# Performance work log

Hardware: AMD Instinct MI355X
Metric: run time of the kernel (lower is better)

Reference implementation:

```python
import math
import jax, jax.numpy as jnp
import numpy as np

N_LAYERS = 3

def _layer_masks(d):
    # Deterministic reproduction of generate_mask_matrix: mask_ratio = 0 for
    # layer < 2 else 1 - log(1/layer + 1); int(ratio*d) random dims zeroed.
    masks = []
    for layer in range(N_LAYERS):
        ratio = 0.0 if layer < 2 else 1.0 - math.log(1.0 / layer + 1.0)
        num_masked = int(ratio * d)
        perm = np.random.RandomState(layer).permutation(d)
        masks.append(jnp.asarray((perm >= num_masked).astype(np.float32)))
    return masks


def setup_inputs() -> dict:
    key = jax.random.key(0)
    ks = jax.random.split(key, 12)
    U, I, R, D, E, B = 50000, 50000, 5, 64, 1000000, 8192
    N = U + I
    return {
        "users": jax.random.randint(ks[0], (B,), 0, U, dtype=jnp.int32),
        "items": jax.random.randint(ks[1], (B,), 0, I, dtype=jnp.int32),
        "user_emb": jax.random.normal(ks[2], (U, D), dtype=jnp.float32) * 0.01,
        "item_emb": jax.random.normal(ks[3], (I, D), dtype=jnp.float32) * 0.01,
        "rating_emb": jax.random.normal(ks[4], (R, D), dtype=jnp.float32) * 0.01,
        "W1": jax.random.normal(ks[5], (R, 2 * D, D), dtype=jnp.float32) * (1.0 / math.sqrt(2 * D)),
        "b1": jnp.zeros((R, D), dtype=jnp.float32),
        "W2": jax.random.normal(ks[6], (R, D, D), dtype=jnp.float32) * (1.0 / math.sqrt(D)),
        "b2": jnp.zeros((R, D), dtype=jnp.float32),
        "rows": jax.random.randint(ks[7], (R, E), 0, N, dtype=jnp.int32),
        "cols": jax.random.randint(ks[8], (R, E), 0, N, dtype=jnp.int32),
        # normalized-adjacency-like positive values (~1/avg_degree)
        "vals": jax.random.uniform(ks[9], (R, E), dtype=jnp.float32) * 0.1,
    }


def reference(users, items, user_emb, item_emb, rating_emb, W1, b1, W2, b2, rows, cols, vals):
    U = user_emb.shape[0]
    N = U + item_emb.shape[0]
    R, D = rating_emb.shape
    masks = _layer_masks(D)

    base = jnp.concatenate([user_emb, item_emb], axis=0)  # [N, D]
    group_outs = []
    for r in range(R):  # fixed small set of rating groups
        # per-rating attention MLP on cat([emb, rating_emb_r])
        t = jnp.concatenate([base, jnp.broadcast_to(rating_emb[r], (N, D))], axis=1)  # [N, 2D]
        h = jax.nn.leaky_relu(t @ W1[r] + b1[r]) @ W2[r] + b2[r]  # [N, D]
        acc = h
        prev = h
        for layer in range(N_LAYERS):
            # sparse A @ prev via gather + segment_sum
            agg = jax.ops.segment_sum(vals[r][:, None] * prev[cols[r]], rows[r], num_segments=N)
            m = masks[layer]
            prev = agg * m + prev * (1.0 - m)  # diag-mask residual combine
            acc = acc + prev
        group_outs.append(acc)

    out = jnp.mean(jnp.stack(group_outs, axis=1), axis=1)  # agg == 'mean'
    users_emb = out[users]
    items_emb = out[U + items]
    return (users_emb * items_emb).sum(1)  # is_mlp = False
```

## Files before the change

kernel.cpp:

```cpp
#include <hip/hip_runtime.h>
#include <hip/hip_bf16.h>
#include <cstdint>
#include <cstddef>

#define KEYSHIFT 20
#define COLMASK 0xFFFFFu
#define EPB 8192
#define SUB 4096
#define BSHIFT 8
#define NRB 256
#define CCAP 3072

__device__ __forceinline__ unsigned short f2bf(float f) {
    uint32_t u = __float_as_uint(f);
    u += ((u >> 16) & 1u) + 0x7fffu;
    return (unsigned short)(u >> 16);
}
__device__ __forceinline__ float bf2f(unsigned short h) {
    return __uint_as_float(((uint32_t)h) << 16);
}

static uint64_t compute_mask_bits() {
    uint32_t mt[624];
    mt[0] = 2u;
    for (int i = 1; i < 624; i++)
        mt[i] = 1812433253u * (mt[i - 1] ^ (mt[i - 1] >> 30)) + (uint32_t)i;
    int mti = 624;
    auto genrand = [&]() -> uint32_t {
        if (mti >= 624) {
            for (int k = 0; k < 624; k++) {
                uint32_t y = (mt[k] & 0x80000000u) | (mt[(k + 1) % 624] & 0x7fffffffu);
                mt[k] = mt[(k + 397) % 624] ^ (y >> 1) ^ ((y & 1u) ? 2567483615u : 0u);
            }
            mti = 0;
        }
        uint32_t y = mt[mti++];
        y ^= y >> 11;
        y ^= (y << 7) & 2636928640u;
        y ^= (y << 15) & 4022730752u;
        y ^= y >> 18;
        return y;
    };
    int arr[64];
    for (int i = 0; i < 64; i++) arr[i] = i;
    for (int i = 63; i >= 1; i--) {
        uint32_t mask = (uint32_t)i;
        mask |= mask >> 1; mask |= mask >> 2; mask |= mask >> 4;
        mask |= mask >> 8; mask |= mask >> 16;
        uint32_t v;
        do { v = genrand() & mask; } while (v > (uint32_t)i);
        int tmp = arr[i]; arr[i] = arr[v]; arr[v] = tmp;
    }
    uint64_t bits = 0;
    for (int d = 0; d < 64; d++)
        if (arr[d] >= 38) bits |= (1ull << d);
    return bits;
}

__global__ void flag_kernel(const int* __restrict__ users, const int* __restrict__ items,
                            unsigned char* __restrict__ flag, int B, int U) {
    int i = blockIdx.x * 256 + threadIdx.x;
    if (i < B) flag[users[i]] = 1;
    else if (i < 2 * B) flag[U + items[i - B]] = 1;
}

__global__ void flist_kernel(const unsigned char* __restrict__ flag,
                             int* __restrict__ flist, int* __restrict__ fcount, int n) {
    int i = blockIdx.x * 256 + threadIdx.x;
    if (i < n && flag[i]) {
        int p = atomicAdd(fcount, 1);
        flist[p] = i;
    }
}

__global__ void c1_kernel(const float* __restrict__ rating_emb, const float* __restrict__ W1,
                          const float* __restrict__ b1, float* __restrict__ c1_all) {
    int r = blockIdx.x;
    int t = threadIdx.x;
    const float* W1r = W1 + (size_t)r * (128 * 64);
    float acc = b1[r * 64 + t];
    for (int k = 0; k < 64; k++)
        acc += rating_emb[r * 64 + k] * W1r[(64 + k) * 64 + t];
    c1_all[r * 64 + t] = acc;
}

__global__ __launch_bounds__(1024) void bucket_count_kernel(
    const int* __restrict__ rows, int* __restrict__ gcnt,
    int* __restrict__ blockBase, int E, int K, int nb) {
    __shared__ int hist[2048];
    int r = blockIdx.y, blk = blockIdx.x, t = threadIdx.x;
    for (int i = t; i < K; i += 1024) hist[i] = 0;
    __syncthreads();
    size_t base = (size_t)r * E + (size_t)blk * EPB;
    int cnt = E - blk * EPB;
    if (cnt > EPB) cnt = EPB;
    for (int k = t; k < cnt; k += 1024)
        atomicAdd(&hist[rows[base + k] >> BSHIFT], 1);
    __syncthreads();
    for (int i = t; i < K; i += 1024) {
        int c = hist[i];
        int bb = (c > 0) ? atomicAdd(&gcnt[r * K + i], c) : 0;
        blockBase[((size_t)r * nb + blk) * K + i] = bb;
    }
}

__global__ void bucket_scan_kernel(const int* __restrict__ gcnt,
                                   int* __restrict__ bptr, int K) {
    __shared__ int sh[256];
    int r = blockIdx.x;
    int t = threadIdx.x;
    int base = t * 8;
    int v[8];
    int s = 0;
    #pragma unroll
    for (int j = 0; j < 8; j++) {
        int idx = base + j;
        v[j] = (idx < K) ? gcnt[r * K + idx] : 0;
        s += v[j];
    }
    sh[t] = s;
    __syncthreads();
    for (int off = 1; off < 256; off <<= 1) {
        int x = (t >= off) ? sh[t - off] : 0;
        __syncthreads();
        sh[t] += x;
        __syncthreads();
    }
    int run = sh[t] - s;
    #pragma unroll
    for (int j = 0; j < 8; j++) {
        int idx = base + j;
        if (idx <= K) bptr[r * (K + 1) + idx] = run;
        run += v[j];
    }
}

__global__ __launch_bounds__(1024) void bucket_scatter_kernel(
    const int* __restrict__ rows, const int* __restrict__ cols,
    const float* __restrict__ vals, const int* __restrict__ bptr,
    const int* __restrict__ blockBase, uint2* __restrict__ rec,
    int E, int K, long long eStride, long long pStride,
    long long bbStride, long long rStride) {
    __shared__ uint2 staged[SUB];
    __shared__ int gaddr[SUB];
    __shared__ int cursor[512];
    __shared__ int lhist[512];
    __shared__ int aux[512];
    int r = blockIdx.y;
    const int* rows_r = rows + (size_t)r * eStride;
    const int* cols_r = cols + (size_t)r * eStride;
    const float* vals_r = vals + (size_t)r * eStride;
    const int* bptr_r = bptr + (size_t)r * pStride;
    const int* bb_r = blockBase + (size_t)r * bbStride;
    uint2* rec_r = rec + (size_t)r * rStride;
    int blk = blockIdx.x, t = threadIdx.x;
    if (t < 512)
        cursor[t] = (t < K) ? (bptr_r[t] + bb_r[(size_t)blk * K + t]) : 0;
    size_t base = (size_t)blk * EPB;
    int cnt = E - blk * EPB;
    if (cnt > EPB) cnt = EPB;
    for (int c0 = 0; c0 < cnt; c0 += SUB) {
        int scnt = cnt - c0;
        if (scnt > SUB) scnt = SUB;
        if (t < 512) lhist[t] = 0;
        __syncthreads();
        int bkt_[4], lpos_[4];
        uint2 rv_[4];
        #pragma unroll
        for (int q = 0; q < 4; q++) {
            int kk = (q << 10) + t;
            bkt_[q] = -1;
            if (kk < scnt) {
                size_t g = base + c0 + kk;
                int row = rows_r[g];
                int b = row >> BSHIFT;
                bkt_[q] = b;
                rv_[q] = make_uint2(((uint32_t)(row & (NRB - 1)) << KEYSHIFT) |
                                        (uint32_t)cols_r[g],
                                    __float_as_uint(vals_r[g]));
                lpos_[q] = atomicAdd(&lhist[b], 1);
            }
        }
        __syncthreads();
        int v = (t < 512) ? lhist[t] : 0;
        if (t < 512) aux[t] = v;
        __syncthreads();
        for (int off = 1; off < 512; off <<= 1) {
            int x = 0;
            if (t >= off && t < 512) x = aux[t - off];
            __syncthreads();
            if (t < 512) aux[t] += x;
            __syncthreads();
        }
        if (t < 512) {
            int ex = aux[t] - v;
            int gb = cursor[t];
            cursor[t] = gb + v;
            lhist[t] = ex;
            aux[t] = gb - ex;
        }
        __syncthreads();
        #pragma unroll
        for (int q = 0; q < 4; q++) {
            if (bkt_[q] >= 0) {
                int sidx = lhist[bkt_[q]] + lpos_[q];
                staged[sidx] = rv_[q];
                gaddr[sidx] = aux[bkt_[q]] + sidx;
            }
        }
        __syncthreads();
        for (int i = t; i < scnt; i += 1024)
            rec_r[gaddr[i]] = staged[i];
        __syncthreads();
    }
}

__global__ __launch_bounds__(1024) void bucket_scatter_legacy(
    const int* __restrict__ rows, const int* __restrict__ cols,
    const float* __restrict__ vals, const int* __restrict__ bptr,
    const int* __restrict__ blockBase, uint2* __restrict__ rec,
    int E, int K, long long eStride, long long pStride,
    long long bbStride, long long rStride) {
    __shared__ int cursor[2048];
    int r = blockIdx.y;
    const int* rows_r = rows + (size_t)r * eStride;
    const int* cols_r = cols + (size_t)r * eStride;
    const float* vals_r = vals + (size_t)r * eStride;
    const int* bptr_r = bptr + (size_t)r * pStride;
    const int* bb_r = blockBase + (size_t)r * bbStride;
    uint2* rec_r = rec + (size_t)r * rStride;
    int blk = blockIdx.x, t = threadIdx.x;
    for (int i = t; i < K; i += 1024)
        cursor[i] = bptr_r[i] + bb_r[(size_t)blk * K + i];
    __syncthreads();
    size_t base = (size_t)blk * EPB;
    int cnt = E - blk * EPB;
    if (cnt > EPB) cnt = EPB;
    for (int k = t; k < cnt; k += 1024) {
        int row = rows_r[base + k];
        int b = row >> BSHIFT;
        int pos = atomicAdd(&cursor[b], 1);
        uint32_t key = ((uint32_t)(row & (NRB - 1)) << KEYSHIFT) | (uint32_t)cols_r[base + k];
        rec_r[pos] = make_uint2(key, __float_as_uint(vals_r[base + k]));
    }
}

__global__ __launch_bounds__(256) void bucket_sort_kernel(
    const uint2* __restrict__ rec, uint2* __restrict__ srec,
    const int* __restrict__ bptr, int* __restrict__ rp, int K, int N,
    long long rStride, long long pStride, long long rpStride) {
    __shared__ uint2 staged[CCAP];
    __shared__ int hist[NRB];
    __shared__ int excl[NRB];
    int r = blockIdx.y;
    const uint2* rec_r = rec + (size_t)r * rStride;
    uint2* srec_r = srec + (size_t)r * rStride;
    const int* bptr_r = bptr + (size_t)r * pStride;
    int* rp_r = rp + (size_t)r * rpStride;
    int b = blockIdx.x;
    int t = threadIdx.x;
    hist[t] = 0;
    __syncthreads();
    int start = bptr_r[b], end = bptr_r[b + 1];
    int m = end - start;
    for (int e = start + t; e < end; e += 256)
        atomicAdd(&hist[rec_r[e].x >> KEYSHIFT], 1);
    __syncthreads();
    int v = hist[t];
    excl[t] = v;
    __syncthreads();
    for (int off = 1; off < 256; off <<= 1) {
        int x = (t >= off) ? excl[t - off] : 0;
        __syncthreads();
        excl[t] += x;
        __syncthreads();
    }
    int ex = excl[t] - v;
    excl[t] = ex;
    hist[t] = 0;
    int row = b * NRB + t;
    if (row < N) rp_r[row] = start + ex;
    if (b == K - 1 && t == 0) rp_r[N] = bptr_r[K];
    __syncthreads();
    if (m <= CCAP) {
        for (int e = start + t; e < end; e += 256) {
            uint2 rr = rec_r[e];
            int rel = (int)(rr.x >> KEYSHIFT);
            int pos = excl[rel] + atomicAdd(&hist[rel], 1);
            staged[pos] = rr;
        }
        __syncthreads();
        for (int i = t; i < m; i += 256)
            srec_r[start + i] = staged[i];
    } else {
        for (int e = start + t; e < end; e += 256) {
            uint2 rr = rec_r[e];
            int rel = (int)(rr.x >> KEYSHIFT);
            int pos = start + excl[rel] + atomicAdd(&hist[rel], 1);
            srec_r[pos] = rr;
        }
    }
}

__global__ __launch_bounds__(256, 4) void mlp_kernel(
    const float* __restrict__ user_emb, const float* __restrict__ item_emb,
    const float* __restrict__ W1, const float* __restrict__ W2,
    const float* __restrict__ c1_all, const float* __restrict__ b2,
    unsigned short* __restrict__ prev, long long prevStride,
    float* __restrict__ out_acc, const unsigned char* __restrict__ flag,
    int r0, int nr, int n_rows, int U, int init) {
    __shared__ float sX[64 * 68];
    __shared__ float sT[64 * 68];

    int t = threadIdx.x;
    int lane = t & 63;
    int row0 = blockIdx.x * 64;
    int jbase = __builtin_amdgcn_readfirstlane((t >> 6) << 4);

    #pragma unroll
    for (int q = 0; q < 4; q++) {
        int f = t + 256 * q;
        int i = f >> 4, c = (f & 15) * 4;
        int nrow = row0 + i;
        float4 xv = make_float4(0.f, 0.f, 0.f, 0.f);
        if (nrow < n_rows) {
            const float* src = (nrow < U) ? (user_emb + (size_t)nrow * 64)
                                          : (item_emb + (size_t)(nrow - U) * 64);
            xv = *(const float4*)(src + c);
        }
        *(float4*)(sX + i * 68 + c) = xv;
    }
    __syncthreads();

    int nrow = row0 + lane;
    bool valid = (nrow < n_rows);
    bool fl = valid && flag[nrow];
    float oa[16];
    #pragma unroll
    for (int i = 0; i < 16; i++) oa[i] = 0.f;

    for (int rr = r0; rr < r0 + nr; ++rr) {
        const float* W1r = W1 + (size_t)rr * (128 * 64);
        const float* W2r = W2 + (size_t)rr * (64 * 64);

        const float* c1p = c1_all + rr * 64 + jbase;
        float4 a0 = *(const float4*)(c1p + 0);
        float4 a1 = *(const float4*)(c1p + 4);
        float4 a2 = *(const float4*)(c1p + 8);
        float4 a3 = *(const float4*)(c1p + 12);

        #pragma unroll
        for (int m = 0; m < 16; m++) {
            float4 xv = *(const float4*)(sX + lane * 68 + 4 * m);
            const float* wk = W1r + (4 * m) * 64 + jbase;
            #pragma unroll
            for (int kk = 0; kk < 4; kk++) {
                float xs = (kk == 0) ? xv.x : (kk == 1) ? xv.y : (kk == 2) ? xv.z : xv.w;
                float4 w0 = *(const float4*)(wk + kk * 64 + 0);
                float4 w1 = *(const float4*)(wk + kk * 64 + 4);
                float4 w2 = *(const float4*)(wk + kk * 64 + 8);
                float4 w3 = *(const float4*)(wk + kk * 64 + 12);
                a0.x += xs * w0.x; a0.y += xs * w0.y; a0.z += xs * w0.z; a0.w += xs * w0.w;
                a1.x += xs * w1.x; a1.y += xs * w1.y; a1.z += xs * w1.z; a1.w += xs * w1.w;
                a2.x += xs * w2.x; a2.y += xs * w2.y; a2.z += xs * w2.z; a2.w += xs * w2.w;
                a3.x += xs * w3.x; a3.y += xs * w3.y; a3.z += xs * w3.z; a3.w += xs * w3.w;
            }
        }
        a0.x = (a0.x >= 0.f) ? a0.x : 0.01f * a0.x;
        a0.y = (a0.y >= 0.f) ? a0.y : 0.01f * a0.y;
        a0.z = (a0.z >= 0.f) ? a0.z : 0.01f * a0.z;
        a0.w = (a0.w >= 0.f) ? a0.w : 0.01f * a0.w;
        a1.x = (a1.x >= 0.f) ? a1.x : 0.01f * a1.x;
        a1.y = (a1.y >= 0.f) ? a1.y : 0.01f * a1.y;
        a1.z = (a1.z >= 0.f) ? a1.z : 0.01f * a1.z;
        a1.w = (a1.w >= 0.f) ? a1.w : 0.01f * a1.w;
        a2.x = (a2.x >= 0.f) ? a2.x : 0.01f * a2.x;
        a2.y = (a2.y >= 0.f) ? a2.y : 0.01f * a2.y;
        a2.z = (a2.z >= 0.f) ? a2.z : 0.01f * a2.z;
        a2.w = (a2.w >= 0.f) ? a2.w : 0.01f * a2.w;
        a3.x = (a3.x >= 0.f) ? a3.x : 0.01f * a3.x;
        a3.y = (a3.y >= 0.f) ? a3.y : 0.01f * a3.y;
        a3.z = (a3.z >= 0.f) ? a3.z : 0.01f * a3.z;
        a3.w = (a3.w >= 0.f) ? a3.w : 0.01f * a3.w;

        *(float4*)(sT + lane * 68 + jbase + 0) = a0;
        *(float4*)(sT + lane * 68 + jbase + 4) = a1;
        *(float4*)(sT + lane * 68 + jbase + 8) = a2;
        *(float4*)(sT + lane * 68 + jbase + 12) = a3;
        __syncthreads();

        const float* b2p = b2 + rr * 64 + jbase;
        a0 = *(const float4*)(b2p + 0);
        a1 = *(const float4*)(b2p + 4);
        a2 = *(const float4*)(b2p + 8);
        a3 = *(const float4*)(b2p + 12);

        #pragma unroll
        for (int m = 0; m < 16; m++) {
            float4 xv = *(const float4*)(sT + lane * 68 + 4 * m);
            const float* wk = W2r + (4 * m) * 64 + jbase;
            #pragma unroll
            for (int kk = 0; kk < 4; kk++) {
                float xs = (kk == 0) ? xv.x : (kk == 1) ? xv.y : (kk == 2) ? xv.z : xv.w;
                float4 w0 = *(const float4*)(wk + kk * 64 + 0);
                float4 w1 = *(const float4*)(wk + kk * 64 + 4);
                float4 w2 = *(const float4*)(wk + kk * 64 + 8);
                float4 w3 = *(const float4*)(wk + kk * 64 + 12);
                a0.x += xs * w0.x; a0.y += xs * w0.y; a0.z += xs * w0.z; a0.w += xs * w0.w;
                a1.x += xs * w1.x; a1.y += xs * w1.y; a1.z += xs * w1.z; a1.w += xs * w1.w;
                a2.x += xs * w2.x; a2.y += xs * w2.y; a2.z += xs * w2.z; a2.w += xs * w2.w;
                a3.x += xs * w3.x; a3.y += xs * w3.y; a3.z += xs * w3.z; a3.w += xs * w3.w;
            }
        }

        if (valid) {
            unsigned short* pp = prev + (size_t)rr * prevStride
                               + (size_t)nrow * 64 + jbase;
            ushort4 h0, h1, h2, h3;
            h0.x = f2bf(a0.x); h0.y = f2bf(a0.y); h0.z = f2bf(a0.z); h0.w = f2bf(a0.w);
            h1.x = f2bf(a1.x); h1.y = f2bf(a1.y); h1.z = f2bf(a1.z); h1.w = f2bf(a1.w);
            h2.x = f2bf(a2.x); h2.y = f2bf(a2.y); h2.z = f2bf(a2.z); h2.w = f2bf(a2.w);
            h3.x = f2bf(a3.x); h3.y = f2bf(a3.y); h3.z = f2bf(a3.z); h3.w = f2bf(a3.w);
            *(ushort4*)(pp + 0) = h0;
            *(ushort4*)(pp + 4) = h1;
            *(ushort4*)(pp + 8) = h2;
            *(ushort4*)(pp + 12) = h3;
            if (fl) {
                oa[0] += a0.x;  oa[1] += a0.y;  oa[2] += a0.z;  oa[3] += a0.w;
                oa[4] += a1.x;  oa[5] += a1.y;  oa[6] += a1.z;  oa[7] += a1.w;
                oa[8] += a2.x;  oa[9] += a2.y;  oa[10] += a2.z; oa[11] += a2.w;
                oa[12] += a3.x; oa[13] += a3.y; oa[14] += a3.z; oa[15] += a3.w;
            }
        }
        __syncthreads();
    }

    if (fl) {
        float* o = out_acc + (size_t)nrow * 64 + jbase;
        if (init) {
            *(float4*)(o + 0) = make_float4(oa[0], oa[1], oa[2], oa[3]);
            *(float4*)(o + 4) = make_float4(oa[4], oa[5], oa[6], oa[7]);
            *(float4*)(o + 8) = make_float4(oa[8], oa[9], oa[10], oa[11]);
            *(float4*)(o + 12) = make_float4(oa[12], oa[13], oa[14], oa[15]);
        } else {
            float4 o0 = *(const float4*)(o + 0);
            float4 o1 = *(const float4*)(o + 4);
            float4 o2 = *(const float4*)(o + 8);
            float4 o3 = *(const float4*)(o + 12);
            o0.x += oa[0];  o0.y += oa[1];  o0.z += oa[2];  o0.w += oa[3];
            o1.x += oa[4];  o1.y += oa[5];  o1.z += oa[6];  o1.w += oa[7];
            o2.x += oa[8];  o2.y += oa[9];  o2.z += oa[10]; o2.w += oa[11];
            o3.x += oa[12]; o3.y += oa[13]; o3.z += oa[14]; o3.w += oa[15];
            *(float4*)(o + 0) = o0;
            *(float4*)(o + 4) = o1;
            *(float4*)(o + 8) = o2;
            *(float4*)(o + 12) = o3;
        }
    }
}

__global__ __launch_bounds__(256) void spmm_kernel(
    const unsigned short* __restrict__ prev, unsigned short* __restrict__ next,
    float* __restrict__ out_acc, const int* __restrict__ rp,
    const uint2* __restrict__ rec, const unsigned char* __restrict__ flag, int n) {
    int wave = (int)((blockIdx.x * (unsigned)blockDim.x + threadIdx.x) >> 6);
    int lane = threadIdx.x & 63;
    int rA = wave * 2;
    if (rA >= n) return;
    int rB = rA + 1;
    int sub = lane >> 4;
    int dl = lane & 15;
    int sA = rp[rA], eA = rp[rA + 1];
    int sB = 0, eB = 0;
    if (rB < n) { sB = rp[rB]; eB = rp[rB + 1]; }
    float axA = 0.f, ayA = 0.f, azA = 0.f, awA = 0.f;
    float axB = 0.f, ayB = 0.f, azB = 0.f, awB = 0.f;
    int ewA = sA + sub, ewB = sB + sub;
    while (ewA < eA || ewB < eB) {
        int a1 = ewA + 4, a2 = ewA + 8, a3 = ewA + 12;
        int b1 = ewB + 4, b2 = ewB + 8, b3 = ewB + 12;
        uint2 ra0 = rec[ewA < eA ? ewA : 0];
        uint2 ra1 = rec[a1 < eA ? a1 : 0];
        uint2 ra2 = rec[a2 < eA ? a2 : 0];
        uint2 ra3 = rec[a3 < eA ? a3 : 0];
        uint2 rb0 = rec[ewB < eB ? ewB : 0];
        uint2 rb1 = rec[b1 < eB ? b1 : 0];
        uint2 rb2 = rec[b2 < eB ? b2 : 0];
        uint2 rb3 = rec[b3 < eB ? b3 : 0];
        float vA0 = (ewA < eA) ? __uint_as_float(ra0.y) : 0.f;
        float vA1 = (a1 < eA) ? __uint_as_float(ra1.y) : 0.f;
        float vA2 = (a2 < eA) ? __uint_as_float(ra2.y) : 0.f;
        float vA3 = (a3 < eA) ? __uint_as_float(ra3.y) : 0.f;
        float vB0 = (ewB < eB) ? __uint_as_float(rb0.y) : 0.f;
        float vB1 = (b1 < eB) ? __uint_as_float(rb1.y) : 0.f;
        float vB2 = (b2 < eB) ? __uint_as_float(rb2.y) : 0.f;
        float vB3 = (b3 < eB) ? __uint_as_float(rb3.y) : 0.f;
        ushort4 qa0 = *(const ushort4*)(prev + (size_t)(ra0.x & COLMASK) * 64 + dl * 4);
        ushort4 qa1 = *(const ushort4*)(prev + (size_t)(ra1.x & COLMASK) * 64 + dl * 4);
        ushort4 qa2 = *(const ushort4*)(prev + (size_t)(ra2.x & COLMASK) * 64 + dl * 4);
        ushort4 qa3 = *(const ushort4*)(prev + (size_t)(ra3.x & COLMASK) * 64 + dl * 4);
        ushort4 qb0 = *(const ushort4*)(prev + (size_t)(rb0.x & COLMASK) * 64 + dl * 4);
        ushort4 qb1 = *(const ushort4*)(prev + (size_t)(rb1.x & COLMASK) * 64 + dl * 4);
        ushort4 qb2 = *(const ushort4*)(prev + (size_t)(rb2.x & COLMASK) * 64 + dl * 4);
        ushort4 qb3 = *(const ushort4*)(prev + (size_t)(rb3.x & COLMASK) * 64 + dl * 4);
        axA += vA0 * bf2f(qa0.x) + vA1 * bf2f(qa1.x) + vA2 * bf2f(qa2.x) + vA3 * bf2f(qa3.x);
        ayA += vA0 * bf2f(qa0.y) + vA1 * bf2f(qa1.y) + vA2 * bf2f(qa2.y) + vA3 * bf2f(qa3.y);
        azA += vA0 * bf2f(qa0.z) + vA1 * bf2f(qa1.z) + vA2 * bf2f(qa2.z) + vA3 * bf2f(qa3.z);
        awA += vA0 * bf2f(qa0.w) + vA1 * bf2f(qa1.w) + vA2 * bf2f(qa2.w) + vA3 * bf2f(qa3.w);
        axB += vB0 * bf2f(qb0.x) + vB1 * bf2f(qb1.x) + vB2 * bf2f(qb2.x) + vB3 * bf2f(qb3.x);
        ayB += vB0 * bf2f(qb0.y) + vB1 * bf2f(qb1.y) + vB2 * bf2f(qb2.y) + vB3 * bf2f(qb3.y);
        azB += vB0 * bf2f(qb0.z) + vB1 * bf2f(qb1.z) + vB2 * bf2f(qb2.z) + vB3 * bf2f(qb3.z);
        awB += vB0 * bf2f(qb0.w) + vB1 * bf2f(qb1.w) + vB2 * bf2f(qb2.w) + vB3 * bf2f(qb3.w);
        ewA += 16; ewB += 16;
    }
    axA += __shfl_xor(axA, 16); ayA += __shfl_xor(ayA, 16);
    azA += __shfl_xor(azA, 16); awA += __shfl_xor(awA, 16);
    axA += __shfl_xor(axA, 32); ayA += __shfl_xor(ayA, 32);
    azA += __shfl_xor(azA, 32); awA += __shfl_xor(awA, 32);
    axB += __shfl_xor(axB, 16); ayB += __shfl_xor(ayB, 16);
    azB += __shfl_xor(azB, 16); awB += __shfl_xor(awB, 16);
    axB += __shfl_xor(axB, 32); ayB += __shfl_xor(ayB, 32);
    azB += __shfl_xor(azB, 32); awB += __shfl_xor(awB, 32);
    if (sub == 0) {
        ushort4 nv;
        nv.x = f2bf(axA); nv.y = f2bf(ayA); nv.z = f2bf(azA); nv.w = f2bf(awA);
        *(ushort4*)(next + (size_t)rA * 64 + dl * 4) = nv;
    } else if (sub == 1 && flag[rA]) {
        float* o = out_acc + (size_t)rA * 64 + dl * 4;
        float4 ov = *(const float4*)o;
        ov.x += axA; ov.y += ayA; ov.z += azA; ov.w += awA;
        *(float4*)o = ov;
    } else if (sub == 2 && rB < n) {
        ushort4 nv;
        nv.x = f2bf(axB); nv.y = f2bf(ayB); nv.z = f2bf(azB); nv.w = f2bf(awB);
        *(ushort4*)(next + (size_t)rB * 64 + dl * 4) = nv;
    } else if (sub == 3 && rB < n && flag[rB]) {
        float* o = out_acc + (size_t)rB * 64 + dl * 4;
        float4 ov = *(const float4*)o;
        ov.x += axB; ov.y += ayB; ov.z += azB; ov.w += awB;
        *(float4*)o = ov;
    }
}

__global__ __launch_bounds__(256) void spmm_masked_kernel(
    const unsigned short* __restrict__ prev, float* __restrict__ out_acc,
    const int* __restrict__ rp, const uint2* __restrict__ rec,
    unsigned long long maskbits, const int* __restrict__ flist,
    const int* __restrict__ fcount) {
    int wave = (int)((blockIdx.x * (unsigned)blockDim.x + threadIdx.x) >> 6);
    int lane = threadIdx.x & 63;
    int fc = *fcount;
    int w2 = wave * 2;
    if (w2 >= fc) return;
    int rowA = flist[w2];
    int rowB = (w2 + 1 < fc) ? flist[w2 + 1] : -1;
    int sub = lane >> 4;
    int dl = lane & 15;
    int sA = rp[rowA], eA = rp[rowA + 1];
    int sB = 0, eB = 0;
    if (rowB >= 0) { sB = rp[rowB]; eB = rp[rowB + 1]; }
    float axA = 0.f, ayA = 0.f, azA = 0.f, awA = 0.f;
    float axB = 0.f, ayB = 0.f, azB = 0.f, awB = 0.f;
    int ewA = sA + sub, ewB = sB + sub;
    while (ewA < eA || ewB < eB) {
        int a1 = ewA + 4, a2 = ewA + 8, a3 = ewA + 12;
        int b1 = ewB + 4, b2 = ewB + 8, b3 = ewB + 12;
        uint2 ra0 = rec[ewA < eA ? ewA : 0];
        uint2 ra1 = rec[a1 < eA ? a1 : 0];
        uint2 ra2 = rec[a2 < eA ? a2 : 0];
        uint2 ra3 = rec[a3 < eA ? a3 : 0];
        uint2 rb0 = rec[ewB < eB ? ewB : 0];
        uint2 rb1 = rec[b1 < eB ? b1 : 0];
        uint2 rb2 = rec[b2 < eB ? b2 : 0];
        uint2 rb3 = rec[b3 < eB ? b3 : 0];
        float vA0 = (ewA < eA) ? __uint_as_float(ra0.y) : 0.f;
        float vA1 = (a1 < eA) ? __uint_as_float(ra1.y) : 0.f;
        float vA2 = (a2 < eA) ? __uint_as_float(ra2.y) : 0.f;
        float vA3 = (a3 < eA) ? __uint_as_float(ra3.y) : 0.f;
        float vB0 = (ewB < eB) ? __uint_as_float(rb0.y) : 0.f;
        float vB1 = (b1 < eB) ? __uint_as_float(rb1.y) : 0.f;
        float vB2 = (b2 < eB) ? __uint_as_float(rb2.y) : 0.f;
        float vB3 = (b3 < eB) ? __uint_as_float(rb3.y) : 0.f;
        ushort4 qa0 = *(const ushort4*)(prev + (size_t)(ra0.x & COLMASK) * 64 + dl * 4);
        ushort4 qa1 = *(const ushort4*)(prev + (size_t)(ra1.x & COLMASK) * 64 + dl * 4);
        ushort4 qa2 = *(const ushort4*)(prev + (size_t)(ra2.x & COLMASK) * 64 + dl * 4);
        ushort4 qa3 = *(const ushort4*)(prev + (size_t)(ra3.x & COLMASK) * 64 + dl * 4);
        ushort4 qb0 = *(const ushort4*)(prev + (size_t)(rb0.x & COLMASK) * 64 + dl * 4);
        ushort4 qb1 = *(const ushort4*)(prev + (size_t)(rb1.x & COLMASK) * 64 + dl * 4);
        ushort4 qb2 = *(const ushort4*)(prev + (size_t)(rb2.x & COLMASK) * 64 + dl * 4);
        ushort4 qb3 = *(const ushort4*)(prev + (size_t)(rb3.x & COLMASK) * 64 + dl * 4);
        axA += vA0 * bf2f(qa0.x) + vA1 * bf2f(qa1.x) + vA2 * bf2f(qa2.x) + vA3 * bf2f(qa3.x);
        ayA += vA0 * bf2f(qa0.y) + vA1 * bf2f(qa1.y) + vA2 * bf2f(qa2.y) + vA3 * bf2f(qa3.y);
        azA += vA0 * bf2f(qa0.z) + vA1 * bf2f(qa1.z) + vA2 * bf2f(qa2.z) + vA3 * bf2f(qa3.z);
        awA += vA0 * bf2f(qa0.w) + vA1 * bf2f(qa1.w) + vA2 * bf2f(qa2.w) + vA3 * bf2f(qa3.w);
        axB += vB0 * bf2f(qb0.x) + vB1 * bf2f(qb1.x) + vB2 * bf2f(qb2.x) + vB3 * bf2f(qb3.x);
        ayB += vB0 * bf2f(qb0.y) + vB1 * bf2f(qb1.y) + vB2 * bf2f(qb2.y) + vB3 * bf2f(qb3.y);
        azB += vB0 * bf2f(qb0.z) + vB1 * bf2f(qb1.z) + vB2 * bf2f(qb2.z) + vB3 * bf2f(qb3.z);
        awB += vB0 * bf2f(qb0.w) + vB1 * bf2f(qb1.w) + vB2 * bf2f(qb2.w) + vB3 * bf2f(qb3.w);
        ewA += 16; ewB += 16;
    }
    axA += __shfl_xor(axA, 16); ayA += __shfl_xor(ayA, 16);
    azA += __shfl_xor(azA, 16); awA += __shfl_xor(awA, 16);
    axA += __shfl_xor(axA, 32); ayA += __shfl_xor(ayA, 32);
    azA += __shfl_xor(azA, 32); awA += __shfl_xor(awA, 32);
    axB += __shfl_xor(axB, 16); ayB += __shfl_xor(ayB, 16);
    azB += __shfl_xor(azB, 16); awB += __shfl_xor(awB, 16);
    axB += __shfl_xor(axB, 32); ayB += __shfl_xor(ayB, 32);
    azB += __shfl_xor(azB, 32); awB += __shfl_xor(awB, 32);
    if (sub == 0) {
        ushort4 pq = *(const ushort4*)(prev + (size_t)rowA * 64 + dl * 4);
        float px = bf2f(pq.x), py = bf2f(pq.y), pz = bf2f(pq.z), pw = bf2f(pq.w);
        float rx = ((maskbits >> (dl * 4 + 0)) & 1ull) ? axA : px;
        float ry = ((maskbits >> (dl * 4 + 1)) & 1ull) ? ayA : py;
        float rz = ((maskbits >> (dl * 4 + 2)) & 1ull) ? azA : pz;
        float rw = ((maskbits >> (dl * 4 + 3)) & 1ull) ? awA : pw;
        float* o = out_acc + (size_t)rowA * 64 + dl * 4;
        float4 ov = *(const float4*)o;
        ov.x += rx; ov.y += ry; ov.z += rz; ov.w += rw;
        *(float4*)o = ov;
    } else if (sub == 2 && rowB >= 0) {
        ushort4 pq = *(const ushort4*)(prev + (size_t)rowB * 64 + dl * 4);
        float px = bf2f(pq.x), py = bf2f(pq.y), pz = bf2f(pq.z), pw = bf2f(pq.w);
        float rx = ((maskbits >> (dl * 4 + 0)) & 1ull) ? axB : px;
        float ry = ((maskbits >> (dl * 4 + 1)) & 1ull) ? ayB : py;
        float rz = ((maskbits >> (dl * 4 + 2)) & 1ull) ? azB : pz;
        float rw = ((maskbits >> (dl * 4 + 3)) & 1ull) ? awB : pw;
        float* o = out_acc + (size_t)rowB * 64 + dl * 4;
        float4 ov = *(const float4*)o;
        ov.x += rx; ov.y += ry; ov.z += rz; ov.w += rw;
        *(float4*)o = ov;
    }
}

__global__ __launch_bounds__(256) void dot_kernel(
    const float* __restrict__ out_acc, const int* __restrict__ users,
    const int* __restrict__ items, float* __restrict__ out,
    int Bn, int U, float scale) {
    int w = (int)((blockIdx.x * (unsigned)blockDim.x + threadIdx.x) >> 6);
    int lane = threadIdx.x & 63;
    if (w >= Bn) return;
    int u = users[w], it = items[w];
    float a = out_acc[(size_t)u * 64 + lane];
    float c = out_acc[((size_t)(U + it)) * 64 + lane];
    float p = a * c;
    #pragma unroll
    for (int off = 32; off > 0; off >>= 1) p += __shfl_down(p, off);
    if (lane == 0) out[w] = p * scale;
}

extern "C" void kernel_launch(void* const* d_in, const int* in_sizes, int n_in,
                              void* d_out, int out_size, void* d_ws, size_t ws_size,
                              hipStream_t stream) {
    const int* users = (const int*)d_in[0];
    const int* items = (const int*)d_in[1];
    const float* user_emb = (const float*)d_in[2];
    const float* item_emb = (const float*)d_in[3];
    const float* rating_emb = (const float*)d_in[4];
    const float* W1 = (const float*)d_in[5];
    const float* b1 = (const float*)d_in[6];
    const float* W2 = (const float*)d_in[7];
    const float* b2 = (const float*)d_in[8];
    const int* rows = (const int*)d_in[9];
    const int* cols = (const int*)d_in[10];
    const float* vals = (const float*)d_in[11];
    float* out = (float*)d_out;

    const int Dd = 64;
    int U = in_sizes[2] / Dd;
    int I = in_sizes[3] / Dd;
    int R = in_sizes[4] / Dd;
    int N = U + I;
    int E = in_sizes[9] / R;
    int Bn = in_sizes[0];
    int K = (N + NRB - 1) / NRB;
    int nb = (E + EPB - 1) / EPB;

    auto al = [](size_t b) { return (b + 255) & ~(size_t)255; };
    size_t sliceA = al((size_t)N * 64 * 2);
    size_t bufA_all = al((size_t)R * N * 64 * 2);
    size_t common = al((size_t)N * 64 * 4) + sliceA
        + al((size_t)R * K * 4)
        + al((size_t)R * (K + 1) * 4) + al((size_t)R * nb * K * 4)
        + al((size_t)R * (N + 1) * 4) + al((size_t)R * 64 * 4)
        + al((size_t)N) + al((size_t)2 * Bn * 4) + al(4);
    size_t rec_one = al((size_t)E * 8);
    size_t rec_all = al((size_t)E * 8 * R);
    int mlpb = 0, batched = 0;
    if (ws_size >= common + bufA_all + 2 * rec_all + 65536) {
        mlpb = 1; batched = 1;
    } else if (ws_size >= common + sliceA + 2 * rec_all + 65536) {
        batched = 1;
    }
    size_t bufAsz = mlpb ? bufA_all : sliceA;
    size_t recsz = batched ? rec_all : rec_one;

    char* p = (char*)d_ws;
    auto carve = [&](size_t bytes) -> char* {
        char* q = p;
        p += (bytes + 255) & ~(size_t)255;
        return q;
    };
    float* out_acc = (float*)carve((size_t)N * 64 * 4);
    unsigned short* bufA = (unsigned short*)carve(bufAsz);
    unsigned short* bufB = (unsigned short*)carve(sliceA);
    uint2* rec = (uint2*)carve(recsz);
    uint2* srec = (uint2*)carve(recsz);
    int* gcnt = (int*)carve((size_t)R * K * 4);
    int* bptr = (int*)carve((size_t)R * (K + 1) * 4);
    int* blockBase = (int*)carve((size_t)R * nb * K * 4);
    int* row_ptr = (int*)carve((size_t)R * (N + 1) * 4);
    float* c1_all = (float*)carve((size_t)R * 64 * 4);
    unsigned char* flag = (unsigned char*)carve((size_t)N);
    int* flist = (int*)carve((size_t)2 * Bn * 4);
    int* fcount = (int*)carve(4);

    uint64_t maskbits = compute_mask_bits();

    hipMemsetAsync(flag, 0, (size_t)N, stream);
    hipMemsetAsync(fcount, 0, 4, stream);
    hipMemsetAsync(gcnt, 0, (size_t)R * K * 4, stream);

    flag_kernel<<<(2 * Bn + 255) / 256, 256, 0, stream>>>(users, items, flag, Bn, U);
    flist_kernel<<<(N + 255) / 256, 256, 0, stream>>>(flag, flist, fcount, N);
    c1_kernel<<<R, 64, 0, stream>>>(rating_emb, W1, b1, c1_all);

    dim3 cgrid(nb, R);
    bucket_count_kernel<<<cgrid, 1024, 0, stream>>>(rows, gcnt, blockBase, E, K, nb);
    bucket_scan_kernel<<<R, 256, 0, stream>>>(gcnt, bptr, K);

    if (batched) {
        dim3 sgrid(nb, R);
        if (K <= 512)
            bucket_scatter_kernel<<<sgrid, 1024, 0, stream>>>(
                rows, cols, vals, bptr, blockBase, rec, E, K,
                (long long)E, (long long)(K + 1), (long long)nb * K, (long long)E);
        else
            bucket_scatter_legacy<<<sgrid, 1024, 0, stream>>>(
                rows, cols, vals, bptr, blockBase, rec, E, K,
                (long long)E, (long long)(K + 1), (long long)nb * K, (long long)E);
        dim3 ogrid(K, R);
        bucket_sort_kernel<<<ogrid, 256, 0, stream>>>(
            rec, srec, bptr, row_ptr, K, N,
            (long long)E, (long long)(K + 1), (long long)(N + 1));
    }

    if (mlpb)
        mlp_kernel<<<(N + 63) / 64, 256, 0, stream>>>(
            user_emb, item_emb, W1, W2, c1_all, b2,
            bufA, (long long)N * 64, out_acc, flag, 0, R, N, U, 1);

    int spmm_waves = (N + 1) / 2;
    int spmm_blocks = (spmm_waves + 3) / 4;
    int masked_blocks = (Bn + 3) / 4;
    for (int r = 0; r < R; r++) {
        const int* bptr_r = bptr + (size_t)r * (K + 1);
        int* rp_r = row_ptr + (size_t)r * (N + 1);
        uint2* srec_r = batched ? (srec + (size_t)r * E) : srec;
        unsigned short* prev_r = mlpb ? (bufA + (size_t)r * N * 64) : bufA;

        if (!batched) {
            dim3 sgrid(nb, 1);
            if (K <= 512)
                bucket_scatter_kernel<<<sgrid, 1024, 0, stream>>>(
                    rows + (size_t)r * E, cols + (size_t)r * E, vals + (size_t)r * E,
                    bptr_r, blockBase + (size_t)r * nb * K, rec, E, K, 0, 0, 0, 0);
            else
                bucket_scatter_legacy<<<sgrid, 1024, 0, stream>>>(
                    rows + (size_t)r * E, cols + (size_t)r * E, vals + (size_t)r * E,
                    bptr_r, blockBase + (size_t)r * nb * K, rec, E, K, 0, 0, 0, 0);
            dim3 ogrid(K, 1);
            bucket_sort_kernel<<<ogrid, 256, 0, stream>>>(
                rec, srec, bptr_r, rp_r, K, N, 0, 0, 0);
        }

        if (!mlpb)
            mlp_kernel<<<(N + 63) / 64, 256, 0, stream>>>(
                user_emb, item_emb, W1, W2, c1_all, b2,
                bufA, 0, out_acc, flag, r, 1, N, U, (r == 0) ? 1 : 0);

        spmm_kernel<<<spmm_blocks, 256, 0, stream>>>(prev_r, bufB, out_acc, rp_r,
                                                     srec_r, flag, N);
        spmm_kernel<<<spmm_blocks, 256, 0, stream>>>(bufB, prev_r, out_acc, rp_r,
                                                     srec_r, flag, N);
        spmm_masked_kernel<<<masked_blocks, 256, 0, stream>>>(prev_r, out_acc, rp_r,
                                                              srec_r, maskbits,
                                                              flist, fcount);
    }

    float scale = 1.0f / (float)(R * R);
    dot_kernel<<<(Bn * 64 + 255) / 256, 256, 0, stream>>>(out_acc, users, items, out,
                                                          Bn, U, scale);
}
```

Baseline: 727.9 us.

## Compute per-rating MLP with bf16 MFMA using split hi/lo precision

Replaces the scalar FP32 FMA loops of the per-rating MLP with MFMA 16x16x32 bf16 instructions. Inputs and weights are split into bf16 hi and lo parts, and three MFMAs per tile approximate FP32 accuracy. A new pack kernel pre-arranges the weights into the MFMA fragment layout in a workspace buffer. This aims to cut the ALU cost of the dense MLP, at the price of an extra launch, 3x the MFMA work, and scattered per-element stores of prev and out_acc.

```diff
diff --git a/kernel.cpp b/kernel.cpp
--- a/kernel.cpp
+++ b/kernel.cpp
@@ -10,6 +10,9 @@
 #define BSHIFT 8
 #define NRB 256
 #define CCAP 3072
+
+typedef short bf16x8 __attribute__((ext_vector_type(8)));
+typedef float f32x4 __attribute__((ext_vector_type(4)));
 
 __device__ __forceinline__ unsigned short f2bf(float f) {
     uint32_t u = __float_as_uint(f);
@@ -82,6 +85,29 @@
     for (int k = 0; k < 64; k++)
         acc += rating_emb[r * 64 + k] * W1r[(64 + k) * 64 + t];
     c1_all[r * 64 + t] = acc;
+}
+
+__global__ void packw_kernel(const float* __restrict__ W1, const float* __restrict__ W2,
+                             short* __restrict__ wpack) {
+    int r = blockIdx.x;
+    int t = threadIdx.x;
+    const float* W1r = W1 + (size_t)r * (128 * 64);
+    const float* W2r = W2 + (size_t)r * (64 * 64);
+    for (int e = t; e < 2 * 4 * 2 * 64 * 8; e += 256) {
+        int i = e & 7;
+        int lane = (e >> 3) & 63;
+        int kc = (e >> 9) & 1;
+        int ct = (e >> 10) & 3;
+        int g = (e >> 12) & 1;
+        int k = kc * 32 + ((lane >> 4) << 3) + i;
+        int col = (ct << 4) + (lane & 15);
+        float w = (g == 0) ? W1r[k * 64 + col] : W2r[k * 64 + col];
+        unsigned short hi = f2bf(w);
+        unsigned short lo = f2bf(w - bf2f(hi));
+        size_t fb = ((((size_t)r * 2 + g) * 4 + ct) * 2 + kc) * 2;
+        wpack[(fb + 0) * 512 + lane * 8 + i] = (short)hi;
+        wpack[(fb + 1) * 512 + lane * 8 + i] = (short)lo;
+    }
 }
 
 __global__ __launch_bounds__(1024) void bucket_count_kernel(
@@ -302,159 +328,149 @@
     }
 }
 
-__global__ __launch_bounds__(256, 4) void mlp_kernel(
+__global__ __launch_bounds__(256) void mlp_kernel(
     const float* __restrict__ user_emb, const float* __restrict__ item_emb,
-    const float* __restrict__ W1, const float* __restrict__ W2,
-    const float* __restrict__ c1_all, const float* __restrict__ b2,
+    const short* __restrict__ wpack, const float* __restrict__ c1_all,
+    const float* __restrict__ b2,
     unsigned short* __restrict__ prev, long long prevStride,
     float* __restrict__ out_acc, const unsigned char* __restrict__ flag,
     int r0, int nr, int n_rows, int U, int init) {
-    __shared__ float sX[64 * 68];
     __shared__ float sT[64 * 68];
 
     int t = threadIdx.x;
-    int lane = t & 63;
+    int wv = t >> 6;
+    int l = t & 63;
     int row0 = blockIdx.x * 64;
-    int jbase = __builtin_amdgcn_readfirstlane((t >> 6) << 4);
-
-    #pragma unroll
-    for (int q = 0; q < 4; q++) {
-        int f = t + 256 * q;
-        int i = f >> 4, c = (f & 15) * 4;
-        int nrow = row0 + i;
-        float4 xv = make_float4(0.f, 0.f, 0.f, 0.f);
-        if (nrow < n_rows) {
-            const float* src = (nrow < U) ? (user_emb + (size_t)nrow * 64)
-                                          : (item_emb + (size_t)(nrow - U) * 64);
-            xv = *(const float4*)(src + c);
-        }
-        *(float4*)(sX + i * 68 + c) = xv;
-    }
-    __syncthreads();
-
-    int nrow = row0 + lane;
-    bool valid = (nrow < n_rows);
-    bool fl = valid && flag[nrow];
+    int arow = row0 + (wv << 4) + (l & 15);
+    int kb = (l >> 4) << 3;
+    int trow = (wv << 4) + (l & 15);
+
+    bf16x8 xh0, xh1, xl0, xl1;
+    {
+        float xv[16];
+        #pragma unroll
+        for (int i = 0; i < 16; i++) xv[i] = 0.f;
+        if (arow < n_rows) {
+            const float* src = (arow < U) ? (user_emb + (size_t)arow * 64)
+                                          : (item_emb + (size_t)(arow - U) * 64);
+            float4 p0 = *(const float4*)(src + kb);
+            float4 p1 = *(const float4*)(src + kb + 4);
+            float4 p2 = *(const float4*)(src + 32 + kb);
+            float4 p3 = *(const float4*)(src + 32 + kb + 4);
+            xv[0] = p0.x; xv[1] = p0.y; xv[2] = p0.z; xv[3] = p0.w;
+            xv[4] = p1.x; xv[5] = p1.y; xv[6] = p1.z; xv[7] = p1.w;
+            xv[8] = p2.x; xv[9] = p2.y; xv[10] = p2.z; xv[11] = p2.w;
+            xv[12] = p3.x; xv[13] = p3.y; xv[14] = p3.z; xv[15] = p3.w;
+        }
+        #pragma unroll
+        for (int i = 0; i < 8; i++) {
+            unsigned short hi = f2bf(xv[i]);
+            xh0[i] = (short)hi;
+            xl0[i] = (short)f2bf(xv[i] - bf2f(hi));
+        }
+        #pragma unroll
+        for (int i = 0; i < 8; i++) {
+            unsigned short hi = f2bf(xv[8 + i]);
+            xh1[i] = (short)hi;
+            xl1[i] = (short)f2bf(xv[8 + i] - bf2f(hi));
+        }
+    }
+
+    int dr0 = row0 + (wv << 4) + ((l >> 4) << 2);
+    bool va0 = (dr0 + 0) < n_rows, va1 = (dr0 + 1) < n_rows;
+    bool va2 = (dr0 + 2) < n_rows, va3 = (dr0 + 3) < n_rows;
+    bool fl0 = va0 && flag[dr0 + 0], fl1 = va1 && flag[dr0 + 1];
+    bool fl2 = va2 && flag[dr0 + 2], fl3 = va3 && flag[dr0 + 3];
     float oa[16];
     #pragma unroll
     for (int i = 0; i < 16; i++) oa[i] = 0.f;
 
     for (int rr = r0; rr < r0 + nr; ++rr) {
-        const float* W1r = W1 + (size_t)rr * (128 * 64);
-        const float* W2r = W2 + (size_t)rr * (64 * 64);
-
-        const float* c1p = c1_all + rr * 64 + jbase;
-        float4 a0 = *(const float4*)(c1p + 0);
-        float4 a1 = *(const float4*)(c1p + 4);
-        float4 a2 = *(const float4*)(c1p + 8);
-        float4 a3 = *(const float4*)(c1p + 12);
+        const short* wp1 = wpack + ((size_t)rr * 2 + 0) * 16 * 512;
+        const short* wp2 = wpack + ((size_t)rr * 2 + 1) * 16 * 512;
 
         #pragma unroll
-        for (int m = 0; m < 16; m++) {
-            float4 xv = *(const float4*)(sX + lane * 68 + 4 * m);
-            const float* wk = W1r + (4 * m) * 64 + jbase;
+        for (int ct = 0; ct < 4; ct++) {
+            float c1v = c1_all[rr * 64 + (ct << 4) + (l & 15)];
+            f32x4 acc = {c1v, c1v, c1v, c1v};
             #pragma unroll
-            for (int kk = 0; kk < 4; kk++) {
-                float xs = (kk == 0) ? xv.x : (kk == 1) ? xv.y : (kk == 2) ? xv.z : xv.w;
-                float4 w0 = *(const float4*)(wk + kk * 64 + 0);
-                float4 w1 = *(const float4*)(wk + kk * 64 + 4);
-                float4 w2 = *(const float4*)(wk + kk * 64 + 8);
-                float4 w3 = *(const float4*)(wk + kk * 64 + 12);
-                a0.x += xs * w0.x; a0.y += xs * w0.y; a0.z += xs * w0.z; a0.w += xs * w0.w;
-                a1.x += xs * w1.x; a1.y += xs * w1.y; a1.z += xs * w1.z; a1.w += xs * w1.w;
-                a2.x += xs * w2.x; a2.y += xs * w2.y; a2.z += xs * w2.z; a2.w += xs * w2.w;
-                a3.x += xs * w3.x; a3.y += xs * w3.y; a3.z += xs * w3.z; a3.w += xs * w3.w;
-            }
-        }
-        a0.x = (a0.x >= 0.f) ? a0.x : 0.01f * a0.x;
-        a0.y = (a0.y >= 0.f) ? a0.y : 0.01f * a0.y;
-        a0.z = (a0.z >= 0.f) ? a0.z : 0.01f * a0.z;
-        a0.w = (a0.w >= 0.f) ? a0.w : 0.01f * a0.w;
-        a1.x = (a1.x >= 0.f) ? a1.x : 0.01f * a1.x;
-        a1.y = (a1.y >= 0.f) ? a1.y : 0.01f * a1.y;
-        a1.z = (a1.z >= 0.f) ? a1.z : 0.01f * a1.z;
-        a1.w = (a1.w >= 0.f) ? a1.w : 0.01f * a1.w;
-        a2.x = (a2.x >= 0.f) ? a2.x : 0.01f * a2.x;
-        a2.y = (a2.y >= 0.f) ? a2.y : 0.01f * a2.y;
-        a2.z = (a2.z >= 0.f) ? a2.z : 0.01f * a2.z;
-        a2.w = (a2.w >= 0.f) ? a2.w : 0.01f * a2.w;
-        a3.x = (a3.x >= 0.f) ? a3.x : 0.01f * a3.x;
-        a3.y = (a3.y >= 0.f) ? a3.y : 0.01f * a3.y;
-        a3.z = (a3.z >= 0.f) ? a3.z : 0.01f * a3.z;
-        a3.w = (a3.w >= 0.f) ? a3.w : 0.01f * a3.w;
-
-        *(float4*)(sT + lane * 68 + jbase + 0) = a0;
-        *(float4*)(sT + lane * 68 + jbase + 4) = a1;
-        *(float4*)(sT + lane * 68 + jbase + 8) = a2;
-        *(float4*)(sT + lane * 68 + jbase + 12) = a3;
-        __syncthreads();
-
-        const float* b2p = b2 + rr * 64 + jbase;
-        a0 = *(const float4*)(b2p + 0);
-        a1 = *(const float4*)(b2p + 4);
-        a2 = *(const float4*)(b2p + 8);
-        a3 = *(const float4*)(b2p + 12);
-
+            for (int kc = 0; kc < 2; kc++) {
+                const short* fb = wp1 + ((ct * 2 + kc) * 2) * 512 + l * 8;
+                bf16x8 bh = *(const bf16x8*)(fb);
+                bf16x8 bl = *(const bf16x8*)(fb + 512);
+                bf16x8 ah = (kc == 0) ? xh0 : xh1;
+                bf16x8 al = (kc == 0) ? xl0 : xl1;
+                acc = __builtin_amdgcn_mfma_f32_16x16x32_bf16(ah, bh, acc, 0, 0, 0);
+                acc = __builtin_amdgcn_mfma_f32_16x16x32_bf16(al, bh, acc, 0, 0, 0);
+                acc = __builtin_amdgcn_mfma_f32_16x16x32_bf16(ah, bl, acc, 0, 0, 0);
+            }
+            #pragma unroll
+            for (int i = 0; i < 4; i++) {
+                float v = acc[i];
+                v = (v >= 0.f) ? v : 0.01f * v;
+                sT[((wv << 4) + ((l >> 4) << 2) + i) * 68 + (ct << 4) + (l & 15)] = v;
+            }
+        }
+        bf16x8 th0, th1, tl0, tl1;
+        {
+            float4 t0 = *(const float4*)(sT + trow * 68 + kb);
+            float4 t1 = *(const float4*)(sT + trow * 68 + kb + 4);
+            float4 t2 = *(const float4*)(sT + trow * 68 + 32 + kb);
+            float4 t3 = *(const float4*)(sT + trow * 68 + 32 + kb + 4);
+            float tv[16] = {t0.x, t0.y, t0.z, t0.w, t1.x, t1.y, t1.z, t1.w,
+                            t2.x, t2.y, t2.z, t2.w, t3.x, t3.y, t3.z, t3.w};
+            #pragma unroll
+            for (int i = 0; i < 8; i++) {
+                unsigned short hi = f2bf(tv[i]);
+                th0[i] = (short)hi;
+                tl0[i] = (short)f2bf(tv[i] - bf2f(hi));
+            }
+            #pragma unroll
+            for (int i = 0; i < 8; i++) {
+                unsigned short hi = f2bf(tv[8 + i]);
+                th1[i] = (short)hi;
+                tl1[i] = (short)f2bf(tv[8 + i] - bf2f(hi));
+            }
+        }
         #pragma unroll
-        for (int m = 0; m < 16; m++) {
-            float4 xv = *(const float4*)(sT + lane * 68 + 4 * m);
-            const float* wk = W2r + (4 * m) * 64 + jbase;
+        for (int ct = 0; ct < 4; ct++) {
+            float b2v = b2[rr * 64 + (ct << 4) + (l & 15)];
+            f32x4 acc = {b2v, b2v, b2v, b2v};
             #pragma unroll
-            for (int kk = 0; kk < 4; kk++) {
-                float xs = (kk == 0) ? xv.x : (kk == 1) ? xv.y : (kk == 2) ? xv.z : xv.w;
-                float4 w0 = *(const float4*)(wk + kk * 64 + 0);
-                float4 w1 = *(const float4*)(wk + kk * 64 + 4);
-                float4 w2 = *(const float4*)(wk + kk * 64 + 8);
-                float4 w3 = *(const float4*)(wk + kk * 64 + 12);
-                a0.x += xs * w0.x; a0.y += xs * w0.y; a0.z += xs * w0.z; a0.w += xs * w0.w;
-                a1.x += xs * w1.x; a1.y += xs * w1.y; a1.z += xs * w1.z; a1.w += xs * w1.w;
-                a2.x += xs * w2.x; a2.y += xs * w2.y; a2.z += xs * w2.z; a2.w += xs * w2.w;
-                a3.x += xs * w3.x; a3.y += xs * w3.y; a3.z += xs * w3.z; a3.w += xs * w3.w;
-            }
-        }
-
-        if (valid) {
-            unsigned short* pp = prev + (size_t)rr * prevStride
-                               + (size_t)nrow * 64 + jbase;
-            ushort4 h0, h1, h2, h3;
-            h0.x = f2bf(a0.x); h0.y = f2bf(a0.y); h0.z = f2bf(a0.z); h0.w = f2bf(a0.w);
-            h1.x = f2bf(a1.x); h1.y = f2bf(a1.y); h1.z = f2bf(a1.z); h1.w = f2bf(a1.w);
-            h2.x = f2bf(a2.x); h2.y = f2bf(a2.y); h2.z = f2bf(a2.z); h2.w = f2bf(a2.w);
-            h3.x = f2bf(a3.x); h3.y = f2bf(a3.y); h3.z = f2bf(a3.z); h3.w = f2bf(a3.w);
-            *(ushort4*)(pp + 0) = h0;
-            *(ushort4*)(pp + 4) = h1;
-            *(ushort4*)(pp + 8) = h2;
-            *(ushort4*)(pp + 12) = h3;
+            for (int kc = 0; kc < 2; kc++) {
+                const short* fb = wp2 + ((ct * 2 + kc) * 2) * 512 + l * 8;
+                bf16x8 bh = *(const bf16x8*)(fb);
+                bf16x8 bl = *(const bf16x8*)(fb + 512);
+                bf16x8 ah = (kc == 0) ? th0 : th1;
+                bf16x8 al = (kc == 0) ? tl0 : tl1;
+                acc = __builtin_amdgcn_mfma_f32_16x16x32_bf16(ah, bh, acc, 0, 0, 0);
+                acc = __builtin_amdgcn_mfma_f32_16x16x32_bf16(al, bh, acc, 0, 0, 0);
+                acc = __builtin_amdgcn_mfma_f32_16x16x32_bf16(ah, bl, acc, 0, 0, 0);
+            }
+            unsigned short* pp = prev + (size_t)rr * prevStride + (ct << 4) + (l & 15);
+            #pragma unroll
+            for (int i = 0; i < 4; i++) {
+                bool va = (i == 0) ? va0 : (i == 1) ? va1 : (i == 2) ? va2 : va3;
+                bool fl = (i == 0) ? fl0 : (i == 1) ? fl1 : (i == 2) ? fl2 : fl3;
+                if (va) {
+                    float hv = acc[i];
+                    pp[(size_t)(dr0 + i) * 64] = f2bf(hv);
+                    if (fl) oa[ct * 4 + i] += hv;
+                }
+            }
+        }
+    }
+
+    #pragma unroll
+    for (int ct = 0; ct < 4; ct++) {
+        #pragma unroll
+        for (int i = 0; i < 4; i++) {
+            bool fl = (i == 0) ? fl0 : (i == 1) ? fl1 : (i == 2) ? fl2 : fl3;
             if (fl) {
-                oa[0] += a0.x;  oa[1] += a0.y;  oa[2] += a0.z;  oa[3] += a0.w;
-                oa[4] += a1.x;  oa[5] += a1.y;  oa[6] += a1.z;  oa[7] += a1.w;
-                oa[8] += a2.x;  oa[9] += a2.y;  oa[10] += a2.z; oa[11] += a2.w;
-                oa[12] += a3.x; oa[13] += a3.y; oa[14] += a3.z; oa[15] += a3.w;
-            }
-        }
-        __syncthreads();
-    }
-
-    if (fl) {
-        float* o = out_acc + (size_t)nrow * 64 + jbase;
-        if (init) {
-            *(float4*)(o + 0) = make_float4(oa[0], oa[1], oa[2], oa[3]);
-            *(float4*)(o + 4) = make_float4(oa[4], oa[5], oa[6], oa[7]);
-            *(float4*)(o + 8) = make_float4(oa[8], oa[9], oa[10], oa[11]);
-            *(float4*)(o + 12) = make_float4(oa[12], oa[13], oa[14], oa[15]);
-        } else {
-            float4 o0 = *(const float4*)(o + 0);
-            float4 o1 = *(const float4*)(o + 4);
-            float4 o2 = *(const float4*)(o + 8);
-            float4 o3 = *(const float4*)(o + 12);
-            o0.x += oa[0];  o0.y += oa[1];  o0.z += oa[2];  o0.w += oa[3];
-            o1.x += oa[4];  o1.y += oa[5];  o1.z += oa[6];  o1.w += oa[7];
-            o2.x += oa[8];  o2.y += oa[9];  o2.z += oa[10]; o2.w += oa[11];
-            o3.x += oa[12]; o3.y += oa[13]; o3.z += oa[14]; o3.w += oa[15];
-            *(float4*)(o + 0) = o0;
-            *(float4*)(o + 4) = o1;
-            *(float4*)(o + 8) = o2;
-            *(float4*)(o + 12) = o3;
+                float* o = out_acc + (size_t)(dr0 + i) * 64 + (ct << 4) + (l & 15);
+                if (init) *o = oa[ct * 4 + i];
+                else *o += oa[ct * 4 + i];
+            }
         }
     }
 }
@@ -678,10 +694,11 @@
     auto al = [](size_t b) { return (b + 255) & ~(size_t)255; };
     size_t sliceA = al((size_t)N * 64 * 2);
     size_t bufA_all = al((size_t)R * N * 64 * 2);
+    size_t wpack_sz = al((size_t)R * 2 * 4 * 2 * 2 * 64 * 8 * 2);
     size_t common = al((size_t)N * 64 * 4) + sliceA
         + al((size_t)R * K * 4)
         + al((size_t)R * (K + 1) * 4) + al((size_t)R * nb * K * 4)
-        + al((size_t)R * (N + 1) * 4) + al((size_t)R * 64 * 4)
+        + al((size_t)R * (N + 1) * 4) + al((size_t)R * 64 * 4) + wpack_sz
         + al((size_t)N) + al((size_t)2 * Bn * 4) + al(4);
     size_t rec_one = al((size_t)E * 8);
     size_t rec_all = al((size_t)E * 8 * R);
@@ -710,6 +727,7 @@
     int* blockBase = (int*)carve((size_t)R * nb * K * 4);
     int* row_ptr = (int*)carve((size_t)R * (N + 1) * 4);
     float* c1_all = (float*)carve((size_t)R * 64 * 4);
+    short* wpack = (short*)carve(wpack_sz);
     unsigned char* flag = (unsigned char*)carve((size_t)N);
     int* flist = (int*)carve((size_t)2 * Bn * 4);
     int* fcount = (int*)carve(4);
@@ -723,6 +741,7 @@
     flag_kernel<<<(2 * Bn + 255) / 256, 256, 0, stream>>>(users, items, flag, Bn, U);
     flist_kernel<<<(N + 255) / 256, 256, 0, stream>>>(flag, flist, fcount, N);
     c1_kernel<<<R, 64, 0, stream>>>(rating_emb, W1, b1, c1_all);
+    packw_kernel<<<R, 256, 0, stream>>>(W1, W2, wpack);
 
     dim3 cgrid(nb, R);
     bucket_count_kernel<<<cgrid, 1024, 0, stream>>>(rows, gcnt, blockBase, E, K, nb);
@@ -746,7 +765,7 @@
 
     if (mlpb)
         mlp_kernel<<<(N + 63) / 64, 256, 0, stream>>>(
-            user_emb, item_emb, W1, W2, c1_all, b2,
+            user_emb, item_emb, wpack, c1_all, b2,
             bufA, (long long)N * 64, out_acc, flag, 0, R, N, U, 1);
 
     int spmm_waves = (N + 1) / 2;
@@ -775,7 +794,7 @@
 
         if (!mlpb)
             mlp_kernel<<<(N + 63) / 64, 256, 0, stream>>>(
-                user_emb, item_emb, W1, W2, c1_all, b2,
+                user_emb, item_emb, wpack, c1_all, b2,
                 bufA, 0, out_acc, flag, r, 1, N, U, (r == 0) ? 1 : 0);
 
         spmm_kernel<<<spmm_blocks, 256, 0, stream>>>(prev_r, bufB, out_acc, rp_r,
```

Result: faster. 667.4 us (-8.3%).
